# Kernel optimization log

Measured on AMD Instinct MI355X. Metric: run time of the kernel, lower is better.

The kernel has to match this reference:

```python
import jax, jax.numpy as jnp
import numpy as np

N_NODES = 50000
N_EDGES = 600000
F_IN = 64
N_GRAPHS = 2000
OUT_DIM = 1
BN_EPS = 1e-5


def _bn(x, gamma, beta):
    # BatchNorm1d training-mode forward: biased batch stats over node/row dim
    m = jnp.mean(x, axis=0)
    v = jnp.var(x, axis=0)
    return (x - m) * jax.lax.rsqrt(v + BN_EPS) * gamma + beta


def _gcn(x, W, b, src, dst):
    # PyG GCNConv: h = x @ W; symmetric-normalized aggregation with self-loops; bias after agg
    n = x.shape[0]
    h = x @ W                                    # [N, C_out]
    ones = jnp.ones((src.shape[0],), h.dtype)
    deg = jax.ops.segment_sum(ones, dst, num_segments=n) + 1.0  # +1 self-loop
    dinv = jax.lax.rsqrt(deg)
    norm = (dinv[src] * dinv[dst])[:, None]      # [E, 1]
    agg = jax.ops.segment_sum(h[src] * norm, dst, num_segments=n)
    agg = agg + h * (1.0 / deg)[:, None]         # self-loop term: deg^{-1/2}*deg^{-1/2}
    return agg + b


def _pool_mean(x, batch, g):
    s = jax.ops.segment_sum(x, batch, num_segments=g)
    c = jax.ops.segment_sum(jnp.ones((x.shape[0],), x.dtype), batch, num_segments=g)
    return s / jnp.maximum(c, 1.0)[:, None]


def _forward(xc, xs, W1c, b1c, g1c, be1c, W2c, b2c, g2c, be2c,
             W1s, b1s, g1s, be1s, W2s, b2s, g2s, be2s,
             Wf1, bf1, gf1, bef1, Wf2, bf2,
             src_c, dst_c, src_s, dst_s, batch):
    hc = jax.nn.relu(_bn(_gcn(xc, W1c, b1c, src_c, dst_c), g1c, be1c))
    hc = jax.nn.relu(_bn(_gcn(hc, W2c, b2c, src_c, dst_c), g2c, be2c))
    hs = jax.nn.relu(_bn(_gcn(xs, W1s, b1s, src_s, dst_s), g1s, be1s))
    hs = jax.nn.relu(_bn(_gcn(hs, W2s, b2s, src_s, dst_s), g2s, be2s))
    pc = _pool_mean(hc, batch, N_GRAPHS)         # [G, 64]
    ps = _pool_mean(hs, batch, N_GRAPHS)         # [G, 64]
    h = jnp.concatenate([pc, ps], axis=1)        # [G, 128]
    h = jax.nn.relu(_bn(h @ Wf1 + bf1, gf1, bef1))  # dropout is identity in eval
    return h @ Wf2 + bf2                         # [G, OUT_DIM]


def setup_inputs() -> dict:
    key = jax.random.key(0)
    ks = jax.random.split(key, 16)

    def glorot(k, fan_in, fan_out):
        s = np.sqrt(2.0 / (fan_in + fan_out)).astype(np.float32)
        return jax.random.normal(k, (fan_in, fan_out), jnp.float32) * s

    inp = {
        'x_chromophore': jax.random.normal(ks[0], (N_NODES, F_IN), jnp.float32),
        'x_solvent': jax.random.normal(ks[1], (N_NODES, F_IN), jnp.float32),
        'edge_index_chromophore': jax.random.randint(ks[2], (2, N_EDGES), 0, N_NODES),
        'edge_index_solvent': jax.random.randint(ks[3], (2, N_EDGES), 0, N_NODES),
        'batch': jnp.sort(jax.random.randint(ks[4], (N_NODES,), 0, N_GRAPHS)),
        # chromophore branch params
        'W1c': glorot(ks[5], F_IN, 128), 'b1c': jnp.zeros((128,), jnp.float32),
        'g1c': jnp.ones((128,), jnp.float32), 'be1c': jnp.zeros((128,), jnp.float32),
        'W2c': glorot(ks[6], 128, 64), 'b2c': jnp.zeros((64,), jnp.float32),
        'g2c': jnp.ones((64,), jnp.float32), 'be2c': jnp.zeros((64,), jnp.float32),
        # solvent branch params
        'W1s': glorot(ks[7], F_IN, 128), 'b1s': jnp.zeros((128,), jnp.float32),
        'g1s': jnp.ones((128,), jnp.float32), 'be1s': jnp.zeros((128,), jnp.float32),
        'W2s': glorot(ks[8], 128, 64), 'b2s': jnp.zeros((64,), jnp.float32),
        'g2s': jnp.ones((64,), jnp.float32), 'be2s': jnp.zeros((64,), jnp.float32),
        # MLP head
        'Wf1': glorot(ks[9], 128, 64), 'bf1': jnp.zeros((64,), jnp.float32),
        'gf1': jnp.ones((64,), jnp.float32), 'bef1': jnp.zeros((64,), jnp.float32),
        'Wf2': glorot(ks[10], 64, OUT_DIM), 'bf2': jnp.zeros((OUT_DIM,), jnp.float32),
    }
    return inp


def reference(x_chromophore, x_solvent, edge_index_chromophore, edge_index_solvent, batch,
              W1c, b1c, g1c, be1c, W2c, b2c, g2c, be2c,
              W1s, b1s, g1s, be1s, W2s, b2s, g2s, be2s,
              Wf1, bf1, gf1, bef1, Wf2, bf2):
    src_c, dst_c = edge_index_chromophore[0], edge_index_chromophore[1]
    src_s, dst_s = edge_index_solvent[0], edge_index_solvent[1]
    return _forward(x_chromophore, x_solvent,
                    W1c, b1c, g1c, be1c, W2c, b2c, g2c, be2c,
                    W1s, b1s, g1s, be1s, W2s, b2s, g2s, be2s,
                    Wf1, bf1, gf1, bef1, Wf2, bf2,
                    src_c, dst_c, src_s, dst_s, batch)
```

## Files before the change

### kernel.cpp

```cpp
#include <hip/hip_runtime.h>
#include <hip/hip_bf16.h>
#include <cstdint>
#include <cstddef>

#define NN 50000
#define NE 600000
#define NG 2000
#define NBUCK 49
#define SLOTS 16
#define NCHUNK 3125

typedef __attribute__((ext_vector_type(8))) short bf8;
typedef __attribute__((ext_vector_type(4))) float f32x4;

__device__ __forceinline__ unsigned short f2bf(float f) {
    uint32_t u = __float_as_uint(f);
    uint32_t r = (u + 0x7FFFu + ((u >> 16) & 1u)) >> 16;
    return (unsigned short)r;
}
__device__ __forceinline__ float bf2f(unsigned short h) {
    return __uint_as_float(((uint32_t)h) << 16);
}

__global__ __launch_bounds__(256) void conv_bf16_kernel(const float* __restrict__ x0,
                                                        const float* __restrict__ x1,
                                                        unsigned short* __restrict__ out) {
    int b = blockIdx.y;
    const float* x = b ? x1 : x0;
    unsigned short* o = out + (size_t)b * NN * 64;
    int i = (blockIdx.x * 256 + threadIdx.x) * 4;
    if (i + 3 < NN * 64) {
        float4 v = *(const float4*)&x[i];
        ushort4 r = make_ushort4(f2bf(v.x), f2bf(v.y), f2bf(v.z), f2bf(v.w));
        *(ushort4*)&o[i] = r;
    }
}

template<int K, int N>
__global__ __launch_bounds__(256) void pack_w(const float* __restrict__ W0,
                                              const float* __restrict__ W1,
                                              unsigned short* __restrict__ out) {
    int b = blockIdx.y;
    const float* W = b ? W1 : W0;
    unsigned short* o = out + (size_t)b * K * N;
    int idx = blockIdx.x * 256 + threadIdx.x;
    const int total = (N / 16) * (K / 32) * 64;
    if (idx >= total) return;
    int l = idx & 63;
    int th = idx >> 6;
    int h = th % (K / 32);
    int t = th / (K / 32);
    int col = t * 16 + (l & 15);
    int k0 = h * 32 + (l >> 4) * 8;
    ushort4 lo = make_ushort4(f2bf(W[(k0 + 0) * N + col]), f2bf(W[(k0 + 1) * N + col]),
                              f2bf(W[(k0 + 2) * N + col]), f2bf(W[(k0 + 3) * N + col]));
    ushort4 hi = make_ushort4(f2bf(W[(k0 + 4) * N + col]), f2bf(W[(k0 + 5) * N + col]),
                              f2bf(W[(k0 + 6) * N + col]), f2bf(W[(k0 + 7) * N + col]));
    *(ushort4*)&o[idx * 8] = lo;
    *(ushort4*)&o[idx * 8 + 4] = hi;
}

__global__ __launch_bounds__(256) void bucket_hist(const int* __restrict__ d0,
                                                   const int* __restrict__ d1,
                                                   int* __restrict__ bucketCnt, int nE) {
    int b = blockIdx.y;
    const int* dst = b ? d1 : d0;
    __shared__ int h[NBUCK];
    for (int i = threadIdx.x; i < NBUCK; i += 256) h[i] = 0;
    __syncthreads();
    for (int e = blockIdx.x * 256 + threadIdx.x; e < nE; e += gridDim.x * 256)
        atomicAdd(&h[dst[e] >> 10], 1);
    __syncthreads();
    for (int i = threadIdx.x; i < NBUCK; i += 256)
        if (h[i]) atomicAdd(&bucketCnt[b * NBUCK + i], h[i]);
}

__global__ void bucket_scan(const int* __restrict__ bucketCnt,
                            int* __restrict__ bucketOff, int* __restrict__ bucketCur) {
    int b = threadIdx.x;
    if (b < 2) {
        int run = 0;
        for (int i = 0; i < NBUCK; ++i) {
            bucketOff[b * NBUCK + i] = run;
            bucketCur[b * NBUCK + i] = run;
            run += bucketCnt[b * NBUCK + i];
        }
    }
}

__global__ __launch_bounds__(256) void bucket_scatter(const int* __restrict__ s0,
                                                      const int* __restrict__ d0,
                                                      const int* __restrict__ s1,
                                                      const int* __restrict__ d1,
                                                      int* __restrict__ bucketCur,
                                                      uint32_t* __restrict__ bent, int nE) {
    int b = blockIdx.y;
    const int* src = b ? s1 : s0;
    const int* dst = b ? d1 : d0;
    __shared__ int cnt[NBUCK];
    __shared__ int base[NBUCK];
    const int tid = threadIdx.x;
    for (int i = tid; i < NBUCK; i += 256) cnt[i] = 0;
    __syncthreads();

    const int e0 = blockIdx.x * 2048 + tid;
    int bk[8], slot[8];
    uint32_t pay[8];
#pragma unroll
    for (int k = 0; k < 8; ++k) {
        int e = e0 + k * 256;
        if (e < nE) {
            int d = dst[e], s = src[e];
            bk[k] = d >> 10;
            pay[k] = ((uint32_t)(d & 1023) << 16) | (uint32_t)s;
            slot[k] = atomicAdd(&cnt[bk[k]], 1);
        } else bk[k] = -1;
    }
    __syncthreads();
    for (int i = tid; i < NBUCK; i += 256) {
        int c = cnt[i];
        base[i] = c ? atomicAdd(&bucketCur[b * NBUCK + i], c) : 0;
    }
    __syncthreads();
#pragma unroll
    for (int k = 0; k < 8; ++k)
        if (bk[k] >= 0)
            bent[(size_t)b * NE + base[bk[k]] + slot[k]] = pay[k];
}

__global__ __launch_bounds__(256) void csr_build(const uint32_t* __restrict__ bent,
                                                 const int* __restrict__ bucketOff,
                                                 const int* __restrict__ bucketCnt,
                                                 int* __restrict__ row_ptr,
                                                 float* __restrict__ dinv,
                                                 uint16_t* __restrict__ perm) {
    __shared__ int lcnt[1024];
    __shared__ int lcur[1024];
    __shared__ int sscan[256];
    const int bk = blockIdx.x;
    const int b = blockIdx.y;
    const int tid = threadIdx.x;
    const int ebase = bucketOff[b * NBUCK + bk];
    const int ecnt = bucketCnt[b * NBUCK + bk];
    const int node0 = bk << 10;
    const uint32_t* be = bent + (size_t)b * NE + ebase;
    int* rp = row_ptr + b * (NN + 1);
    float* dv = dinv + (size_t)b * NN;
    uint16_t* pm = perm + (size_t)b * NE + ebase;

    for (int i = tid; i < 1024; i += 256) lcnt[i] = 0;
    __syncthreads();
    for (int i = tid; i < ecnt; i += 256) atomicAdd(&lcnt[be[i] >> 16], 1);
    __syncthreads();

    int c[4], s = 0;
#pragma unroll
    for (int j = 0; j < 4; ++j) { c[j] = lcnt[tid * 4 + j]; s += c[j]; }
    sscan[tid] = s;
    __syncthreads();
    for (int off = 1; off < 256; off <<= 1) {
        int v = (tid >= off) ? sscan[tid - off] : 0;
        __syncthreads();
        sscan[tid] += v;
        __syncthreads();
    }
    int run = sscan[tid] - s;
#pragma unroll
    for (int j = 0; j < 4; ++j) {
        int nl = tid * 4 + j;
        int g = node0 + nl;
        if (g < NN) {
            rp[g] = ebase + run;
            lcur[nl] = run;
            dv[g] = rsqrtf((float)c[j] + 1.0f);
        }
        run += c[j];
    }
    if (bk == NBUCK - 1 && tid == 0) rp[NN] = ebase + ecnt;
    __syncthreads();

    for (int i = tid; i < ecnt; i += 256) {
        uint32_t en = be[i];
        int nl = en >> 16;
        int pos = atomicAdd(&lcur[nl], 1);
        pm[pos] = (uint16_t)(en & 0xFFFFu);
    }
}

__global__ __launch_bounds__(256) void weight_fill(const uint16_t* __restrict__ perm,
                                                   const float* __restrict__ dinv,
                                                   uint32_t* __restrict__ permw, int nE) {
    int b = blockIdx.y;
    const uint16_t* pm = perm + (size_t)b * NE;
    const float* dv = dinv + (size_t)b * NN;
    uint32_t* pw = permw + (size_t)b * NE;
    int i = (blockIdx.x * 256 + threadIdx.x) * 4;
    if (i + 3 < nE) {
        ushort4 s4 = *(const ushort4*)&pm[i];
        uint4 o;
        o.x = ((uint32_t)f2bf(dv[s4.x]) << 16) | (uint32_t)s4.x;
        o.y = ((uint32_t)f2bf(dv[s4.y]) << 16) | (uint32_t)s4.y;
        o.z = ((uint32_t)f2bf(dv[s4.z]) << 16) | (uint32_t)s4.z;
        o.w = ((uint32_t)f2bf(dv[s4.w]) << 16) | (uint32_t)s4.w;
        *(uint4*)&pw[i] = o;
    } else {
        for (; i < nE; ++i) {
            uint16_t s = pm[i];
            pw[i] = ((uint32_t)f2bf(dv[s]) << 16) | (uint32_t)s;
        }
    }
}

__global__ __launch_bounds__(256) void gemm1_mfma(const unsigned short* __restrict__ Xbf,
                                                  const unsigned short* __restrict__ Wp,
                                                  unsigned short* __restrict__ Y) {
    const int b = blockIdx.y;
    const unsigned short* __restrict__ X = Xbf + (size_t)b * NN * 64;
    const unsigned short* __restrict__ W = Wp + (size_t)b * 64 * 128;
    unsigned short* __restrict__ Yb = Y + (size_t)b * NN * 128;
    const int tid = threadIdx.x;
    const int w = tid >> 6, lane = tid & 63;
    const int chunk = blockIdx.x * 4 + w;
    if (chunk >= NCHUNK) return;
    const int m = lane & 15, quad = lane >> 4;

    const int row = chunk * 16 + m;
    bf8 a0 = *(const bf8*)&X[(size_t)row * 64 + quad * 8];
    bf8 a1 = *(const bf8*)&X[(size_t)row * 64 + 32 + quad * 8];
    f32x4 acc[8];
#pragma unroll
    for (int t = 0; t < 8; ++t) acc[t] = (f32x4){0.f, 0.f, 0.f, 0.f};
#pragma unroll
    for (int t = 0; t < 8; ++t) {
        bf8 b0 = *(const bf8*)&W[((t * 2 + 0) * 64 + lane) * 8];
        bf8 b1 = *(const bf8*)&W[((t * 2 + 1) * 64 + lane) * 8];
        acc[t] = __builtin_amdgcn_mfma_f32_16x16x32_bf16(b0, a0, acc[t], 0, 0, 0);
        acc[t] = __builtin_amdgcn_mfma_f32_16x16x32_bf16(b1, a1, acc[t], 0, 0, 0);
    }
#pragma unroll
    for (int t = 0; t < 8; ++t) {
        uint32_t lo = (uint32_t)f2bf(acc[t][0]) | ((uint32_t)f2bf(acc[t][1]) << 16);
        uint32_t hi = (uint32_t)f2bf(acc[t][2]) | ((uint32_t)f2bf(acc[t][3]) << 16);
        *(uint2*)&Yb[(size_t)row * 128 + t * 16 + quad * 4] = make_uint2(lo, hi);
    }
}

__global__ __launch_bounds__(256) void stats128_bf16(const unsigned short* __restrict__ Y,
                                                     float* __restrict__ sums) {
    const int b = blockIdx.y;
    const unsigned short* __restrict__ Yb = Y + (size_t)b * NN * 128;
    const int g = threadIdx.x & 31;
    const int rs = threadIdx.x >> 5;
    float s0 = 0.f, s1 = 0.f, s2 = 0.f, s3 = 0.f;
    float q0 = 0.f, q1 = 0.f, q2 = 0.f, q3 = 0.f;
    for (int r = blockIdx.x * 8 + rs; r < NN; r += gridDim.x * 8) {
        uint2 v = *(const uint2*)&Yb[(size_t)r * 128 + g * 4];
        float x0 = __uint_as_float(v.x << 16);
        float x1 = __uint_as_float(v.x & 0xFFFF0000u);
        float x2 = __uint_as_float(v.y << 16);
        float x3 = __uint_as_float(v.y & 0xFFFF0000u);
        s0 += x0; s1 += x1; s2 += x2; s3 += x3;
        q0 = fmaf(x0, x0, q0); q1 = fmaf(x1, x1, q1);
        q2 = fmaf(x2, x2, q2); q3 = fmaf(x3, x3, q3);
    }
    __shared__ float ls[8][128], lq[8][128];
    *(float4*)&ls[rs][g * 4] = make_float4(s0, s1, s2, s3);
    *(float4*)&lq[rs][g * 4] = make_float4(q0, q1, q2, q3);
    __syncthreads();
    if (threadIdx.x < 128) {
        const int c = threadIdx.x;
        float S = 0.f, Q = 0.f;
#pragma unroll
        for (int k = 0; k < 8; ++k) { S += ls[k][c]; Q += lq[k][c]; }
        int slot = blockIdx.x & (SLOTS - 1);
        float* sb = sums + (size_t)(b * SLOTS + slot) * 256;
        atomicAdd(&sb[c], S);
        atomicAdd(&sb[128 + c], Q);
    }
}

__global__ __launch_bounds__(256) void gemm2_mfma(const unsigned short* __restrict__ H1,
                                                  const unsigned short* __restrict__ Wp,
                                                  const float* __restrict__ sums,
                                                  const float* __restrict__ g0,
                                                  const float* __restrict__ g1,
                                                  const float* __restrict__ be0,
                                                  const float* __restrict__ be1,
                                                  unsigned short* __restrict__ Y) {
    __shared__ float scLds[128], shLds[128];
    const int b = blockIdx.y;
    const unsigned short* __restrict__ X = H1 + (size_t)b * NN * 128;
    const unsigned short* __restrict__ W = Wp + (size_t)b * 128 * 64;
    unsigned short* __restrict__ Yb = Y + (size_t)b * NN * 64;
    const int tid = threadIdx.x;

    if (tid < 128) {
        float s = 0.f, s2 = 0.f;
#pragma unroll
        for (int k = 0; k < SLOTS; ++k) {
            const float* sb = sums + (size_t)(b * SLOTS + k) * 256;
            s += sb[tid];
            s2 += sb[128 + tid];
        }
        const float invN = 1.0f / (float)NN;
        float mean = s * invN;
        float var = s2 * invN - mean * mean;
        float gamma = b ? g1[tid] : g0[tid];
        float beta = b ? be1[tid] : be0[tid];
        float sc = gamma * rsqrtf(var + 1e-5f);
        scLds[tid] = sc;
        shLds[tid] = beta - mean * sc;
    }
    __syncthreads();

    const int w = tid >> 6, lane = tid & 63;
    const int chunk = blockIdx.x * 4 + w;
    if (chunk >= NCHUNK) return;
    const int m = lane & 15, quad = lane >> 4;
    const int row = chunk * 16 + m;

    f32x4 acc[4];
#pragma unroll
    for (int t = 0; t < 4; ++t) acc[t] = (f32x4){0.f, 0.f, 0.f, 0.f};
#pragma unroll
    for (int h = 0; h < 4; ++h) {
        const int k0 = h * 32 + quad * 8;
        bf8 araw = *(const bf8*)&X[(size_t)row * 128 + k0];
        float4 sc0 = *(const float4*)&scLds[k0];
        float4 sc1 = *(const float4*)&scLds[k0 + 4];
        float4 sh0 = *(const float4*)&shLds[k0];
        float4 sh1 = *(const float4*)&shLds[k0 + 4];
        float scv[8] = {sc0.x, sc0.y, sc0.z, sc0.w, sc1.x, sc1.y, sc1.z, sc1.w};
        float shv[8] = {sh0.x, sh0.y, sh0.z, sh0.w, sh1.x, sh1.y, sh1.z, sh1.w};
        bf8 af;
#pragma unroll
        for (int j = 0; j < 8; ++j) {
            float v = bf2f((unsigned short)araw[j]);
            v = fmaxf(fmaf(v, scv[j], shv[j]), 0.f);
            af[j] = (short)f2bf(v);
        }
#pragma unroll
        for (int t = 0; t < 4; ++t) {
            bf8 bf = *(const bf8*)&W[((t * 4 + h) * 64 + lane) * 8];
            acc[t] = __builtin_amdgcn_mfma_f32_16x16x32_bf16(bf, af, acc[t], 0, 0, 0);
        }
    }
#pragma unroll
    for (int t = 0; t < 4; ++t) {
        uint32_t lo = (uint32_t)f2bf(acc[t][0]) | ((uint32_t)f2bf(acc[t][1]) << 16);
        uint32_t hi = (uint32_t)f2bf(acc[t][2]) | ((uint32_t)f2bf(acc[t][3]) << 16);
        *(uint2*)&Yb[(size_t)row * 64 + t * 16 + quad * 4] = make_uint2(lo, hi);
    }
}

template<bool STATS>
__global__ __launch_bounds__(256) void agg2_kernel(const unsigned short* __restrict__ hall,
                                                   const int* __restrict__ row_ptr,
                                                   const uint32_t* __restrict__ permw,
                                                   const float* __restrict__ dinv,
                                                   unsigned short* __restrict__ out,
                                                   float* __restrict__ sums, int nNodes) {
    const int b = blockIdx.y;
    const unsigned short* __restrict__ h = hall + (size_t)b * NN * 64;
    const int* rp = row_ptr + b * (NN + 1);
    const uint32_t* pe = permw + (size_t)b * NE;
    const float* dv = dinv + (size_t)b * NN;
    unsigned short* ob = out + (size_t)b * nNodes * 64;

    const int w = threadIdx.x >> 6;
    const int wave = blockIdx.x * 4 + w;
    const int lane = threadIdx.x & 63;
    const int q = lane & 15;
    const int r = lane >> 4;
    float f0 = 0.f, f1 = 0.f, f2 = 0.f, f3 = 0.f;
    const bool active = wave < nNodes;
    if (active) {
        const int d = wave;
        const float di = dv[d];
        const int p0 = rp[d], p1 = rp[d + 1];
        float a0 = 0.f, a1 = 0.f, a2 = 0.f, a3 = 0.f;
        for (int p = p0; p < p1; p += 16) {
            uint32_t en[4];
#pragma unroll
            for (int k = 0; k < 4; ++k) {
                int e = p + k * 4 + r;
                bool vld = e < p1;
                en[k] = pe[vld ? e : p0];
                if (!vld) en[k] &= 0xFFFFu;
            }
#pragma unroll
            for (int k = 0; k < 4; ++k) {
                const int idx = (int)(en[k] & 0xFFFFu);
                const float wk = __uint_as_float(en[k] & 0xFFFF0000u);
                const uint2 hv = *(const uint2*)&h[(size_t)idx * 64 + q * 4];
                a0 = fmaf(wk, __uint_as_float(hv.x << 16), a0);
                a1 = fmaf(wk, __uint_as_float(hv.x & 0xFFFF0000u), a1);
                a2 = fmaf(wk, __uint_as_float(hv.y << 16), a2);
                a3 = fmaf(wk, __uint_as_float(hv.y & 0xFFFF0000u), a3);
            }
        }
        a0 += __shfl_xor(a0, 16, 64); a0 += __shfl_xor(a0, 32, 64);
        a1 += __shfl_xor(a1, 16, 64); a1 += __shfl_xor(a1, 32, 64);
        a2 += __shfl_xor(a2, 16, 64); a2 += __shfl_xor(a2, 32, 64);
        a3 += __shfl_xor(a3, 16, 64); a3 += __shfl_xor(a3, 32, 64);
        const uint2 sv = *(const uint2*)&h[(size_t)d * 64 + q * 4];
        f0 = di * fmaf(di, __uint_as_float(sv.x << 16), a0);
        f1 = di * fmaf(di, __uint_as_float(sv.x & 0xFFFF0000u), a1);
        f2 = di * fmaf(di, __uint_as_float(sv.y << 16), a2);
        f3 = di * fmaf(di, __uint_as_float(sv.y & 0xFFFF0000u), a3);
        if (r == 0) {
            uint32_t o0 = (uint32_t)f2bf(f0) | ((uint32_t)f2bf(f1) << 16);
            uint32_t o1 = (uint32_t)f2bf(f2) | ((uint32_t)f2bf(f3) << 16);
            *(uint2*)&ob[(size_t)d * 64 + q * 4] = make_uint2(o0, o1);
        }
    }
    if constexpr (STATS) {
        __shared__ float ls[256], ls2[256];
        if (lane < 16) {
            *(float4*)&ls[w * 64 + q * 4]  = make_float4(f0, f1, f2, f3);
            *(float4*)&ls2[w * 64 + q * 4] = make_float4(f0 * f0, f1 * f1, f2 * f2, f3 * f3);
        }
        __syncthreads();
        if (threadIdx.x < 64) {
            const int t = threadIdx.x;
            float s  = ls[t]  + ls[t + 64]  + ls[t + 128]  + ls[t + 192];
            float s2 = ls2[t] + ls2[t + 64] + ls2[t + 128] + ls2[t + 192];
            int slot = blockIdx.x & (SLOTS - 1);
            float* sb = sums + ((size_t)(b * SLOTS + slot) * 2) * 64;
            atomicAdd(&sb[t], s);
            atomicAdd(&sb[64 + t], s2);
        }
    }
}

__global__ __launch_bounds__(64) void pool2_kernel(const unsigned short* __restrict__ x,
                                                   const float* __restrict__ sums,
                                                   const float* __restrict__ g0,
                                                   const float* __restrict__ g1,
                                                   const float* __restrict__ be0,
                                                   const float* __restrict__ be1,
                                                   const int* __restrict__ batch,
                                                   float* __restrict__ Hmean, int n) {
    int b = blockIdx.y;
    const unsigned short* xb = x + (size_t)b * NN * 64;
    int g = blockIdx.x;
    int c = threadIdx.x;
    float s0 = 0.f, s20 = 0.f;
#pragma unroll
    for (int k = 0; k < SLOTS; ++k) {
        const float* sb = sums + ((size_t)(b * SLOTS + k) * 2) * 64;
        s0 += sb[c];
        s20 += sb[64 + c];
    }
    const float invN = 1.0f / (float)NN;
    float mean = s0 * invN;
    float var = s20 * invN - mean * mean;
    float gamma = b ? g1[c] : g0[c];
    float beta = b ? be1[c] : be0[c];
    float sc = gamma * rsqrtf(var + 1e-5f);
    float sh = beta - mean * sc;

    int lo = 0, hi = n;
    while (lo < hi) { int mid = (lo + hi) >> 1; if (batch[mid] < g) lo = mid + 1; else hi = mid; }
    int start = lo;
    hi = n;
    while (lo < hi) { int mid = (lo + hi) >> 1; if (batch[mid] <= g) lo = mid + 1; else hi = mid; }
    int end = lo;
    float s = 0.f;
    for (int r = start; r < end; ++r)
        s += fmaxf(fmaf(bf2f(xb[(size_t)r * 64 + c]), sc, sh), 0.f);
    float cf = (float)(end - start);
    Hmean[(size_t)g * 128 + b * 64 + c] = s / fmaxf(cf, 1.f);
}

__global__ __launch_bounds__(64) void head_gemm1_kernel(const float* __restrict__ H,
                                                        const float* __restrict__ Wf1,
                                                        float* __restrict__ T) {
    __shared__ float row[128];
    int g = blockIdx.x;
    int c = threadIdx.x;
    row[c] = H[(size_t)g * 128 + c];
    row[c + 64] = H[(size_t)g * 128 + 64 + c];
    __syncthreads();
    float acc = 0.f;
#pragma unroll 8
    for (int k = 0; k < 128; ++k) acc = fmaf(row[k], Wf1[k * 64 + c], acc);
    T[(size_t)g * 64 + c] = acc;
}

template<int C>
__global__ __launch_bounds__(256) void bn_stats_kernel(const float* __restrict__ x, int n,
                                                       float* __restrict__ sums) {
    constexpr int RP = 256 / C;
    __shared__ float ls[256], ls2[256];
    int c = threadIdx.x % C;
    int sub = threadIdx.x / C;
    float s = 0.f, s2 = 0.f;
    for (int r = blockIdx.x * RP + sub; r < n; r += gridDim.x * RP) {
        float v = x[(size_t)r * C + c];
        s += v; s2 += v * v;
    }
    ls[threadIdx.x] = s; ls2[threadIdx.x] = s2;
    __syncthreads();
    if (sub == 0) {
#pragma unroll
        for (int k = 1; k < RP; ++k) { s += ls[k * C + c]; s2 += ls2[k * C + c]; }
        atomicAdd(&sums[c], s);
        atomicAdd(&sums[C + c], s2);
    }
}

__global__ __launch_bounds__(64) void head_final_kernel(const float* __restrict__ T,
                                                        const float* __restrict__ hsums,
                                                        const float* __restrict__ gf1,
                                                        const float* __restrict__ bef1,
                                                        const float* __restrict__ Wf2,
                                                        const float* __restrict__ bf2,
                                                        float* __restrict__ out) {
    int g = blockIdx.x;
    int c = threadIdx.x;
    const float invG = 1.0f / (float)NG;
    float mean = hsums[c] * invG;
    float var = hsums[64 + c] * invG - mean * mean;
    float sc = gf1[c] * rsqrtf(var + 1e-5f);
    float sh = bef1[c] - mean * sc;
    float v = fmaxf(fmaf(T[(size_t)g * 64 + c], sc, sh), 0.f) * Wf2[c];
#pragma unroll
    for (int off = 32; off > 0; off >>= 1) v += __shfl_down(v, off, 64);
    if (c == 0) out[g] = v + bf2[0];
}


static inline size_t alignup(size_t x) { return (x + 255) & ~(size_t)255; }

extern "C" void kernel_launch(void* const* d_in, const int* in_sizes, int n_in,
                              void* d_out, int out_size, void* d_ws, size_t ws_size,
                              hipStream_t stream) {
    const float* xc  = (const float*)d_in[0];
    const float* xs  = (const float*)d_in[1];
    const int*   eic = (const int*)d_in[2];
    const int*   eis = (const int*)d_in[3];
    const int*   batch = (const int*)d_in[4];
    const float* W1c = (const float*)d_in[5];
    const float* g1c = (const float*)d_in[7];
    const float* be1c = (const float*)d_in[8];
    const float* W2c = (const float*)d_in[9];
    const float* g2c = (const float*)d_in[11];
    const float* be2c = (const float*)d_in[12];
    const float* W1s = (const float*)d_in[13];
    const float* g1s = (const float*)d_in[15];
    const float* be1s = (const float*)d_in[16];
    const float* W2s = (const float*)d_in[17];
    const float* g2s = (const float*)d_in[19];
    const float* be2s = (const float*)d_in[20];
    const float* Wf1 = (const float*)d_in[21];
    const float* gf1 = (const float*)d_in[23];
    const float* bef1 = (const float*)d_in[24];
    const float* Wf2 = (const float*)d_in[25];
    const float* bf2 = (const float*)d_in[26];
    float* out = (float*)d_out;

    char* ws = (char*)d_ws;
    size_t off = 0;
    auto alloc = [&](size_t bytes) { char* p = ws + off; off += alignup(bytes); return p; };

    int*      bucketCnt = (int*)alloc(2 * NBUCK * 4);
    int*      bucketOff = (int*)alloc(2 * NBUCK * 4);
    int*      bucketCur = (int*)alloc(2 * NBUCK * 4);
    uint32_t* bent      = (uint32_t*)alloc((size_t)2 * NE * 4);
    uint16_t* perm      = (uint16_t*)alloc(((size_t)2 * NE + 64) * 2);
    int*      row_ptr   = (int*)alloc(2 * (NN + 1) * 4);
    float*    dinv      = (float*)alloc((size_t)2 * NN * 4);
    unsigned short* xbf   = (unsigned short*)alloc((size_t)2 * NN * 64 * 2);
    unsigned short* aggbf = (unsigned short*)alloc((size_t)2 * NN * 64 * 2);
    unsigned short* h1bf  = (unsigned short*)alloc((size_t)2 * NN * 128 * 2);
    unsigned short* h2bf  = (unsigned short*)alloc((size_t)2 * NN * 64 * 2);
    unsigned short* Wp1   = (unsigned short*)alloc((size_t)2 * 64 * 128 * 2);
    unsigned short* Wp2   = (unsigned short*)alloc((size_t)2 * 128 * 64 * 2);
    float*    sums1     = (float*)alloc(((size_t)2 * SLOTS * 256 + (size_t)2 * SLOTS * 128 + 128) * 4);
    float*    sums2     = sums1 + (size_t)2 * SLOTS * 256;
    float*    hsums     = sums2 + (size_t)2 * SLOTS * 128;
    float*    Hmean     = (float*)alloc((size_t)NG * 128 * 4);
    float*    T         = (float*)alloc((size_t)NG * 64 * 4);

    const size_t statBytes = ((size_t)2 * SLOTS * 256 + (size_t)2 * SLOTS * 128 + 128) * 4;
    const int gemmBlocks = (NCHUNK + 3) / 4;
    const int aggBlocks = (NN + 3) / 4;

    conv_bf16_kernel<<<dim3((NN * 64 / 4 + 255) / 256, 2), 256, 0, stream>>>(xc, xs, xbf);
    pack_w<64, 128><<<dim3(4, 2), 256, 0, stream>>>(W1c, W1s, Wp1);
    pack_w<128, 64><<<dim3(4, 2), 256, 0, stream>>>(W2c, W2s, Wp2);
    hipMemsetAsync(sums1, 0, statBytes, stream);

    hipMemsetAsync(bucketCnt, 0, 2 * NBUCK * 4, stream);
    bucket_hist<<<dim3(64, 2), 256, 0, stream>>>(eic + NE, eis + NE, bucketCnt, NE);
    bucket_scan<<<1, 64, 0, stream>>>(bucketCnt, bucketOff, bucketCur);
    bucket_scatter<<<dim3((NE + 2047) / 2048, 2), 256, 0, stream>>>(
        eic, eic + NE, eis, eis + NE, bucketCur, bent, NE);
    csr_build<<<dim3(NBUCK, 2), 256, 0, stream>>>(bent, bucketOff, bucketCnt,
                                                  row_ptr, dinv, perm);
    weight_fill<<<dim3((NE / 4 + 255) / 256, 2), 256, 0, stream>>>(perm, dinv, bent, NE);

    agg2_kernel<false><<<dim3(aggBlocks, 2), 256, 0, stream>>>(
        xbf, row_ptr, bent, dinv, aggbf, nullptr, NN);
    gemm1_mfma<<<dim3(gemmBlocks, 2), 256, 0, stream>>>(aggbf, Wp1, h1bf);
    stats128_bf16<<<dim3(256, 2), 256, 0, stream>>>(h1bf, sums1);

    gemm2_mfma<<<dim3(gemmBlocks, 2), 256, 0, stream>>>(h1bf, Wp2, sums1,
                                                        g1c, g1s, be1c, be1s, h2bf);
    agg2_kernel<true><<<dim3(aggBlocks, 2), 256, 0, stream>>>(
        h2bf, row_ptr, bent, dinv, aggbf, sums2, NN);

    pool2_kernel<<<dim3(NG, 2), 64, 0, stream>>>(aggbf, sums2, g2c, g2s, be2c, be2s,
                                                 batch, Hmean, NN);

    head_gemm1_kernel<<<NG, 64, 0, stream>>>(Hmean, Wf1, T);
    bn_stats_kernel<64><<<32, 256, 0, stream>>>(T, NG, hsums);
    head_final_kernel<<<NG, 64, 0, stream>>>(T, hsums, gf1, bef1, Wf2, bf2, out);
}
```

Measured before the change: 354.6 us.

## Pad CSR rows to multiples of 16 and widen aggregation gathers to 16-byte loads

Each node's CSR row is padded to a multiple of 16 entries. Padding slots carry a zero weight and index 0, so the aggregation loop needs no bounds checks. Row pointers become (start,end) int2 pairs. The aggregation kernel now has 8 lanes per row, each loading 8 bf16 features with uint4, and 8 rows are gathered per iteration, followed by a three-step shuffle reduction. The cost is extra padded edge storage, padded work in weight_fill and on low-degree nodes, and more serial padding writes in csr_build.

```diff
diff --git a/kernel.cpp b/kernel.cpp
--- a/kernel.cpp
+++ b/kernel.cpp
@@ -9,6 +9,7 @@
 #define NBUCK 49
 #define SLOTS 16
 #define NCHUNK 3125
+#define PNE (NE + NBUCK * 15 * 1024)
 
 typedef __attribute__((ext_vector_type(8))) short bf8;
 typedef __attribute__((ext_vector_type(4))) float f32x4;
@@ -21,6 +22,8 @@
 __device__ __forceinline__ float bf2f(unsigned short h) {
     return __uint_as_float(((uint32_t)h) << 16);
 }
+__device__ __forceinline__ float lo16(uint32_t v) { return __uint_as_float(v << 16); }
+__device__ __forceinline__ float hi16(uint32_t v) { return __uint_as_float(v & 0xFFFF0000u); }
 
 __global__ __launch_bounds__(256) void conv_bf16_kernel(const float* __restrict__ x0,
                                                         const float* __restrict__ x1,
@@ -125,13 +128,13 @@
 #pragma unroll
     for (int k = 0; k < 8; ++k)
         if (bk[k] >= 0)
-            bent[(size_t)b * NE + base[bk[k]] + slot[k]] = pay[k];
+            bent[(size_t)b * (size_t)PNE + base[bk[k]] + slot[k]] = pay[k];
 }
 
 __global__ __launch_bounds__(256) void csr_build(const uint32_t* __restrict__ bent,
                                                  const int* __restrict__ bucketOff,
                                                  const int* __restrict__ bucketCnt,
-                                                 int* __restrict__ row_ptr,
+                                                 int2* __restrict__ rpe,
                                                  float* __restrict__ dinv,
                                                  uint16_t* __restrict__ perm) {
     __shared__ int lcnt[1024];
@@ -142,20 +145,25 @@
     const int tid = threadIdx.x;
     const int ebase = bucketOff[b * NBUCK + bk];
     const int ecnt = bucketCnt[b * NBUCK + bk];
+    const int P0 = ebase + bk * 15360;
     const int node0 = bk << 10;
-    const uint32_t* be = bent + (size_t)b * NE + ebase;
-    int* rp = row_ptr + b * (NN + 1);
+    const uint32_t* be = bent + (size_t)b * (size_t)PNE + ebase;
+    int2* rp = rpe + (size_t)b * NN;
     float* dv = dinv + (size_t)b * NN;
-    uint16_t* pm = perm + (size_t)b * NE + ebase;
+    uint16_t* pm = perm + (size_t)b * (size_t)PNE + P0;
 
     for (int i = tid; i < 1024; i += 256) lcnt[i] = 0;
     __syncthreads();
     for (int i = tid; i < ecnt; i += 256) atomicAdd(&lcnt[be[i] >> 16], 1);
     __syncthreads();
 
-    int c[4], s = 0;
-#pragma unroll
-    for (int j = 0; j < 4; ++j) { c[j] = lcnt[tid * 4 + j]; s += c[j]; }
+    int c[4], pc[4], s = 0;
+#pragma unroll
+    for (int j = 0; j < 4; ++j) {
+        c[j] = lcnt[tid * 4 + j];
+        pc[j] = (c[j] + 15) & ~15;
+        s += pc[j];
+    }
     sscan[tid] = s;
     __syncthreads();
     for (int off = 1; off < 256; off <<= 1) {
@@ -170,13 +178,12 @@
         int nl = tid * 4 + j;
         int g = node0 + nl;
         if (g < NN) {
-            rp[g] = ebase + run;
+            rp[g] = make_int2(P0 + run, P0 + run + pc[j]);
             lcur[nl] = run;
             dv[g] = rsqrtf((float)c[j] + 1.0f);
         }
-        run += c[j];
-    }
-    if (bk == NBUCK - 1 && tid == 0) rp[NN] = ebase + ecnt;
+        run += pc[j];
+    }
     __syncthreads();
 
     for (int i = tid; i < ecnt; i += 256) {
@@ -185,28 +192,38 @@
         int pos = atomicAdd(&lcur[nl], 1);
         pm[pos] = (uint16_t)(en & 0xFFFFu);
     }
+    __syncthreads();
+
+    int run2 = sscan[tid] - s;
+#pragma unroll
+    for (int j = 0; j < 4; ++j) {
+        int g = node0 + tid * 4 + j;
+        if (g < NN)
+            for (int t = c[j]; t < pc[j]; ++t) pm[run2 + t] = 0xFFFFu;
+        run2 += pc[j];
+    }
 }
 
 __global__ __launch_bounds__(256) void weight_fill(const uint16_t* __restrict__ perm,
                                                    const float* __restrict__ dinv,
                                                    uint32_t* __restrict__ permw, int nE) {
     int b = blockIdx.y;
-    const uint16_t* pm = perm + (size_t)b * NE;
+    const uint16_t* pm = perm + (size_t)b * (size_t)PNE;
     const float* dv = dinv + (size_t)b * NN;
-    uint32_t* pw = permw + (size_t)b * NE;
+    uint32_t* pw = permw + (size_t)b * (size_t)PNE;
     int i = (blockIdx.x * 256 + threadIdx.x) * 4;
     if (i + 3 < nE) {
         ushort4 s4 = *(const ushort4*)&pm[i];
         uint4 o;
-        o.x = ((uint32_t)f2bf(dv[s4.x]) << 16) | (uint32_t)s4.x;
-        o.y = ((uint32_t)f2bf(dv[s4.y]) << 16) | (uint32_t)s4.y;
-        o.z = ((uint32_t)f2bf(dv[s4.z]) << 16) | (uint32_t)s4.z;
-        o.w = ((uint32_t)f2bf(dv[s4.w]) << 16) | (uint32_t)s4.w;
+        o.x = (s4.x < NN) ? (((uint32_t)f2bf(dv[s4.x]) << 16) | (uint32_t)s4.x) : 0u;
+        o.y = (s4.y < NN) ? (((uint32_t)f2bf(dv[s4.y]) << 16) | (uint32_t)s4.y) : 0u;
+        o.z = (s4.z < NN) ? (((uint32_t)f2bf(dv[s4.z]) << 16) | (uint32_t)s4.z) : 0u;
+        o.w = (s4.w < NN) ? (((uint32_t)f2bf(dv[s4.w]) << 16) | (uint32_t)s4.w) : 0u;
         *(uint4*)&pw[i] = o;
     } else {
         for (; i < nE; ++i) {
             uint16_t s = pm[i];
-            pw[i] = ((uint32_t)f2bf(dv[s]) << 16) | (uint32_t)s;
+            pw[i] = (s < NN) ? (((uint32_t)f2bf(dv[s]) << 16) | (uint32_t)s) : 0u;
         }
     }
 }
@@ -255,10 +272,10 @@
     float q0 = 0.f, q1 = 0.f, q2 = 0.f, q3 = 0.f;
     for (int r = blockIdx.x * 8 + rs; r < NN; r += gridDim.x * 8) {
         uint2 v = *(const uint2*)&Yb[(size_t)r * 128 + g * 4];
-        float x0 = __uint_as_float(v.x << 16);
-        float x1 = __uint_as_float(v.x & 0xFFFF0000u);
-        float x2 = __uint_as_float(v.y << 16);
-        float x3 = __uint_as_float(v.y & 0xFFFF0000u);
+        float x0 = lo16(v.x);
+        float x1 = hi16(v.x);
+        float x2 = lo16(v.y);
+        float x3 = hi16(v.y);
         s0 += x0; s1 += x1; s2 += x2; s3 += x3;
         q0 = fmaf(x0, x0, q0); q1 = fmaf(x1, x1, q1);
         q2 = fmaf(x2, x2, q2); q3 = fmaf(x3, x3, q3);
@@ -355,70 +372,90 @@
 
 template<bool STATS>
 __global__ __launch_bounds__(256) void agg2_kernel(const unsigned short* __restrict__ hall,
-                                                   const int* __restrict__ row_ptr,
+                                                   const int2* __restrict__ rpe,
                                                    const uint32_t* __restrict__ permw,
                                                    const float* __restrict__ dinv,
                                                    unsigned short* __restrict__ out,
                                                    float* __restrict__ sums, int nNodes) {
     const int b = blockIdx.y;
     const unsigned short* __restrict__ h = hall + (size_t)b * NN * 64;
-    const int* rp = row_ptr + b * (NN + 1);
-    const uint32_t* pe = permw + (size_t)b * NE;
+    const int2* rp = rpe + (size_t)b * NN;
+    const uint32_t* pe = permw + (size_t)b * (size_t)PNE;
     const float* dv = dinv + (size_t)b * NN;
     unsigned short* ob = out + (size_t)b * nNodes * 64;
 
     const int w = threadIdx.x >> 6;
     const int wave = blockIdx.x * 4 + w;
     const int lane = threadIdx.x & 63;
-    const int q = lane & 15;
-    const int r = lane >> 4;
-    float f0 = 0.f, f1 = 0.f, f2 = 0.f, f3 = 0.f;
+    const int g = lane >> 3;
+    const int c = lane & 7;
+    float a0 = 0.f, a1 = 0.f, a2 = 0.f, a3 = 0.f;
+    float a4 = 0.f, a5 = 0.f, a6 = 0.f, a7 = 0.f;
+    float fv[8];
+#pragma unroll
+    for (int j = 0; j < 8; ++j) fv[j] = 0.f;
+
     const bool active = wave < nNodes;
     if (active) {
         const int d = wave;
         const float di = dv[d];
-        const int p0 = rp[d], p1 = rp[d + 1];
-        float a0 = 0.f, a1 = 0.f, a2 = 0.f, a3 = 0.f;
-        for (int p = p0; p < p1; p += 16) {
-            uint32_t en[4];
-#pragma unroll
-            for (int k = 0; k < 4; ++k) {
-                int e = p + k * 4 + r;
-                bool vld = e < p1;
-                en[k] = pe[vld ? e : p0];
-                if (!vld) en[k] &= 0xFFFFu;
-            }
-#pragma unroll
-            for (int k = 0; k < 4; ++k) {
-                const int idx = (int)(en[k] & 0xFFFFu);
-                const float wk = __uint_as_float(en[k] & 0xFFFF0000u);
-                const uint2 hv = *(const uint2*)&h[(size_t)idx * 64 + q * 4];
-                a0 = fmaf(wk, __uint_as_float(hv.x << 16), a0);
-                a1 = fmaf(wk, __uint_as_float(hv.x & 0xFFFF0000u), a1);
-                a2 = fmaf(wk, __uint_as_float(hv.y << 16), a2);
-                a3 = fmaf(wk, __uint_as_float(hv.y & 0xFFFF0000u), a3);
-            }
-        }
-        a0 += __shfl_xor(a0, 16, 64); a0 += __shfl_xor(a0, 32, 64);
-        a1 += __shfl_xor(a1, 16, 64); a1 += __shfl_xor(a1, 32, 64);
-        a2 += __shfl_xor(a2, 16, 64); a2 += __shfl_xor(a2, 32, 64);
-        a3 += __shfl_xor(a3, 16, 64); a3 += __shfl_xor(a3, 32, 64);
-        const uint2 sv = *(const uint2*)&h[(size_t)d * 64 + q * 4];
-        f0 = di * fmaf(di, __uint_as_float(sv.x << 16), a0);
-        f1 = di * fmaf(di, __uint_as_float(sv.x & 0xFFFF0000u), a1);
-        f2 = di * fmaf(di, __uint_as_float(sv.y << 16), a2);
-        f3 = di * fmaf(di, __uint_as_float(sv.y & 0xFFFF0000u), a3);
-        if (r == 0) {
-            uint32_t o0 = (uint32_t)f2bf(f0) | ((uint32_t)f2bf(f1) << 16);
-            uint32_t o1 = (uint32_t)f2bf(f2) | ((uint32_t)f2bf(f3) << 16);
-            *(uint2*)&ob[(size_t)d * 64 + q * 4] = make_uint2(o0, o1);
+        const int2 pr = rp[d];
+        for (int p = pr.x; p < pr.y; p += 16) {
+            const uint32_t e0 = pe[p + g];
+            const uint32_t e1 = pe[p + 8 + g];
+            const int i0 = (int)(e0 & 0xFFFFu);
+            const int i1 = (int)(e1 & 0xFFFFu);
+            const float w0 = __uint_as_float(e0 & 0xFFFF0000u);
+            const float w1 = __uint_as_float(e1 & 0xFFFF0000u);
+            const uint4 v0 = *(const uint4*)&h[(size_t)i0 * 64 + c * 8];
+            const uint4 v1 = *(const uint4*)&h[(size_t)i1 * 64 + c * 8];
+            a0 = fmaf(w0, lo16(v0.x), a0); a1 = fmaf(w0, hi16(v0.x), a1);
+            a2 = fmaf(w0, lo16(v0.y), a2); a3 = fmaf(w0, hi16(v0.y), a3);
+            a4 = fmaf(w0, lo16(v0.z), a4); a5 = fmaf(w0, hi16(v0.z), a5);
+            a6 = fmaf(w0, lo16(v0.w), a6); a7 = fmaf(w0, hi16(v0.w), a7);
+            a0 = fmaf(w1, lo16(v1.x), a0); a1 = fmaf(w1, hi16(v1.x), a1);
+            a2 = fmaf(w1, lo16(v1.y), a2); a3 = fmaf(w1, hi16(v1.y), a3);
+            a4 = fmaf(w1, lo16(v1.z), a4); a5 = fmaf(w1, hi16(v1.z), a5);
+            a6 = fmaf(w1, lo16(v1.w), a6); a7 = fmaf(w1, hi16(v1.w), a7);
+        }
+        a0 += __shfl_xor(a0, 8, 64);  a1 += __shfl_xor(a1, 8, 64);
+        a2 += __shfl_xor(a2, 8, 64);  a3 += __shfl_xor(a3, 8, 64);
+        a4 += __shfl_xor(a4, 8, 64);  a5 += __shfl_xor(a5, 8, 64);
+        a6 += __shfl_xor(a6, 8, 64);  a7 += __shfl_xor(a7, 8, 64);
+        a0 += __shfl_xor(a0, 16, 64); a1 += __shfl_xor(a1, 16, 64);
+        a2 += __shfl_xor(a2, 16, 64); a3 += __shfl_xor(a3, 16, 64);
+        a4 += __shfl_xor(a4, 16, 64); a5 += __shfl_xor(a5, 16, 64);
+        a6 += __shfl_xor(a6, 16, 64); a7 += __shfl_xor(a7, 16, 64);
+        a0 += __shfl_xor(a0, 32, 64); a1 += __shfl_xor(a1, 32, 64);
+        a2 += __shfl_xor(a2, 32, 64); a3 += __shfl_xor(a3, 32, 64);
+        a4 += __shfl_xor(a4, 32, 64); a5 += __shfl_xor(a5, 32, 64);
+        a6 += __shfl_xor(a6, 32, 64); a7 += __shfl_xor(a7, 32, 64);
+
+        if (g == 0) {
+            const uint4 sv = *(const uint4*)&h[(size_t)d * 64 + c * 8];
+            fv[0] = di * fmaf(di, lo16(sv.x), a0);
+            fv[1] = di * fmaf(di, hi16(sv.x), a1);
+            fv[2] = di * fmaf(di, lo16(sv.y), a2);
+            fv[3] = di * fmaf(di, hi16(sv.y), a3);
+            fv[4] = di * fmaf(di, lo16(sv.z), a4);
+            fv[5] = di * fmaf(di, hi16(sv.z), a5);
+            fv[6] = di * fmaf(di, lo16(sv.w), a6);
+            fv[7] = di * fmaf(di, hi16(sv.w), a7);
+            uint4 o;
+            o.x = (uint32_t)f2bf(fv[0]) | ((uint32_t)f2bf(fv[1]) << 16);
+            o.y = (uint32_t)f2bf(fv[2]) | ((uint32_t)f2bf(fv[3]) << 16);
+            o.z = (uint32_t)f2bf(fv[4]) | ((uint32_t)f2bf(fv[5]) << 16);
+            o.w = (uint32_t)f2bf(fv[6]) | ((uint32_t)f2bf(fv[7]) << 16);
+            *(uint4*)&ob[(size_t)d * 64 + c * 8] = o;
         }
     }
     if constexpr (STATS) {
         __shared__ float ls[256], ls2[256];
-        if (lane < 16) {
-            *(float4*)&ls[w * 64 + q * 4]  = make_float4(f0, f1, f2, f3);
-            *(float4*)&ls2[w * 64 + q * 4] = make_float4(f0 * f0, f1 * f1, f2 * f2, f3 * f3);
+        if (g == 0) {
+            *(float4*)&ls[w * 64 + c * 8]      = make_float4(fv[0], fv[1], fv[2], fv[3]);
+            *(float4*)&ls[w * 64 + c * 8 + 4]  = make_float4(fv[4], fv[5], fv[6], fv[7]);
+            *(float4*)&ls2[w * 64 + c * 8]     = make_float4(fv[0]*fv[0], fv[1]*fv[1], fv[2]*fv[2], fv[3]*fv[3]);
+            *(float4*)&ls2[w * 64 + c * 8 + 4] = make_float4(fv[4]*fv[4], fv[5]*fv[5], fv[6]*fv[6], fv[7]*fv[7]);
         }
         __syncthreads();
         if (threadIdx.x < 64) {
@@ -567,9 +604,9 @@
     int*      bucketCnt = (int*)alloc(2 * NBUCK * 4);
     int*      bucketOff = (int*)alloc(2 * NBUCK * 4);
     int*      bucketCur = (int*)alloc(2 * NBUCK * 4);
-    uint32_t* bent      = (uint32_t*)alloc((size_t)2 * NE * 4);
-    uint16_t* perm      = (uint16_t*)alloc(((size_t)2 * NE + 64) * 2);
-    int*      row_ptr   = (int*)alloc(2 * (NN + 1) * 4);
+    uint32_t* bent      = (uint32_t*)alloc((size_t)2 * PNE * 4);
+    uint16_t* perm      = (uint16_t*)alloc(((size_t)2 * PNE + 64) * 2);
+    int2*     rpe       = (int2*)alloc((size_t)2 * NN * 8);
     float*    dinv      = (float*)alloc((size_t)2 * NN * 4);
     unsigned short* xbf   = (unsigned short*)alloc((size_t)2 * NN * 64 * 2);
     unsigned short* aggbf = (unsigned short*)alloc((size_t)2 * NN * 64 * 2);
@@ -598,18 +635,18 @@
     bucket_scatter<<<dim3((NE + 2047) / 2048, 2), 256, 0, stream>>>(
         eic, eic + NE, eis, eis + NE, bucketCur, bent, NE);
     csr_build<<<dim3(NBUCK, 2), 256, 0, stream>>>(bent, bucketOff, bucketCnt,
-                                                  row_ptr, dinv, perm);
-    weight_fill<<<dim3((NE / 4 + 255) / 256, 2), 256, 0, stream>>>(perm, dinv, bent, NE);
+                                                  rpe, dinv, perm);
+    weight_fill<<<dim3((PNE / 4 + 255) / 256, 2), 256, 0, stream>>>(perm, dinv, bent, PNE);
 
     agg2_kernel<false><<<dim3(aggBlocks, 2), 256, 0, stream>>>(
-        xbf, row_ptr, bent, dinv, aggbf, nullptr, NN);
+        xbf, rpe, bent, dinv, aggbf, nullptr, NN);
     gemm1_mfma<<<dim3(gemmBlocks, 2), 256, 0, stream>>>(aggbf, Wp1, h1bf);
     stats128_bf16<<<dim3(256, 2), 256, 0, stream>>>(h1bf, sums1);
 
     gemm2_mfma<<<dim3(gemmBlocks, 2), 256, 0, stream>>>(h1bf, Wp2, sums1,
                                                         g1c, g1s, be1c, be1s, h2bf);
     agg2_kernel<true><<<dim3(aggBlocks, 2), 256, 0, stream>>>(
-        h2bf, row_ptr, bent, dinv, aggbf, sums2, NN);
+        h2bf, rpe, bent, dinv, aggbf, sums2, NN);
 
     pool2_kernel<<<dim3(NG, 2), 64, 0, stream>>>(aggbf, sums2, g2c, g2s, be2c, be2s,
                                                  batch, Hmean, NN);
```

Result: no change. 359.2 us (+1.3%).

## Sort CSR neighbor lists in LDS and precompute graph node ranges

Applied to the files above, without the earlier changes.

In csr_build, each bucket's permuted source indices are now staged in a shared-memory buffer. Each thread then insertion-sorts the neighbor lists of its rows before writing them out, which makes the gathers in aggregation read rows in ascending order and should improve cache locality. A new graph_ranges kernel computes start and end node indices per graph once, replacing two binary searches per pool block. The cost is extra serial sorting work in csr_build, a 32KB LDS buffer that can limit occupancy, and an added kernel launch plus memset. The pooling change assumes batch is sorted and treats graphs with no nodes as empty via the memset.

```diff
diff --git a/kernel.cpp b/kernel.cpp
--- a/kernel.cpp
+++ b/kernel.cpp
@@ -21,6 +21,8 @@
 __device__ __forceinline__ float bf2f(unsigned short h) {
     return __uint_as_float(((uint32_t)h) << 16);
 }
+__device__ __forceinline__ float lo16(uint32_t v) { return __uint_as_float(v << 16); }
+__device__ __forceinline__ float hi16(uint32_t v) { return __uint_as_float(v & 0xFFFF0000u); }
 
 __global__ __launch_bounds__(256) void conv_bf16_kernel(const float* __restrict__ x0,
                                                         const float* __restrict__ x1,
@@ -137,6 +139,7 @@
     __shared__ int lcnt[1024];
     __shared__ int lcur[1024];
     __shared__ int sscan[256];
+    __shared__ uint16_t spm[16384];
     const int bk = blockIdx.x;
     const int b = blockIdx.y;
     const int tid = threadIdx.x;
@@ -179,11 +182,31 @@
     if (bk == NBUCK - 1 && tid == 0) rp[NN] = ebase + ecnt;
     __syncthreads();
 
+    const bool useLds = (ecnt <= 16384);
+    uint16_t* dstbuf = useLds ? spm : pm;
     for (int i = tid; i < ecnt; i += 256) {
         uint32_t en = be[i];
         int nl = en >> 16;
         int pos = atomicAdd(&lcur[nl], 1);
-        pm[pos] = (uint16_t)(en & 0xFFFFu);
+        dstbuf[pos] = (uint16_t)(en & 0xFFFFu);
+    }
+    __syncthreads();
+
+    if (useLds) {
+        int st = sscan[tid] - s;
+#pragma unroll
+        for (int j = 0; j < 4; ++j) {
+            const int cnt = c[j];
+            for (int a = st + 1; a < st + cnt; ++a) {
+                uint16_t v = spm[a];
+                int k2 = a - 1;
+                while (k2 >= st && spm[k2] > v) { spm[k2 + 1] = spm[k2]; --k2; }
+                spm[k2 + 1] = v;
+            }
+            st += cnt;
+        }
+        __syncthreads();
+        for (int i = tid; i < ecnt; i += 256) pm[i] = spm[i];
     }
 }
 
@@ -211,6 +234,16 @@
     }
 }
 
+__global__ __launch_bounds__(256) void graph_ranges(const int* __restrict__ batch,
+                                                    int* __restrict__ gstart,
+                                                    int* __restrict__ gend, int n) {
+    int i = blockIdx.x * 256 + threadIdx.x;
+    if (i >= n) return;
+    int g = batch[i];
+    if (i == 0 || batch[i - 1] != g) gstart[g] = i;
+    if (i == n - 1 || batch[i + 1] != g) gend[g] = i + 1;
+}
+
 __global__ __launch_bounds__(256) void gemm1_mfma(const unsigned short* __restrict__ Xbf,
                                                   const unsigned short* __restrict__ Wp,
                                                   unsigned short* __restrict__ Y) {
@@ -255,10 +288,10 @@
     float q0 = 0.f, q1 = 0.f, q2 = 0.f, q3 = 0.f;
     for (int r = blockIdx.x * 8 + rs; r < NN; r += gridDim.x * 8) {
         uint2 v = *(const uint2*)&Yb[(size_t)r * 128 + g * 4];
-        float x0 = __uint_as_float(v.x << 16);
-        float x1 = __uint_as_float(v.x & 0xFFFF0000u);
-        float x2 = __uint_as_float(v.y << 16);
-        float x3 = __uint_as_float(v.y & 0xFFFF0000u);
+        float x0 = lo16(v.x);
+        float x1 = hi16(v.x);
+        float x2 = lo16(v.y);
+        float x3 = hi16(v.y);
         s0 += x0; s1 += x1; s2 += x2; s3 += x3;
         q0 = fmaf(x0, x0, q0); q1 = fmaf(x1, x1, q1);
         q2 = fmaf(x2, x2, q2); q3 = fmaf(x3, x3, q3);
@@ -393,10 +426,10 @@
                 const int idx = (int)(en[k] & 0xFFFFu);
                 const float wk = __uint_as_float(en[k] & 0xFFFF0000u);
                 const uint2 hv = *(const uint2*)&h[(size_t)idx * 64 + q * 4];
-                a0 = fmaf(wk, __uint_as_float(hv.x << 16), a0);
-                a1 = fmaf(wk, __uint_as_float(hv.x & 0xFFFF0000u), a1);
-                a2 = fmaf(wk, __uint_as_float(hv.y << 16), a2);
-                a3 = fmaf(wk, __uint_as_float(hv.y & 0xFFFF0000u), a3);
+                a0 = fmaf(wk, lo16(hv.x), a0);
+                a1 = fmaf(wk, hi16(hv.x), a1);
+                a2 = fmaf(wk, lo16(hv.y), a2);
+                a3 = fmaf(wk, hi16(hv.y), a3);
             }
         }
         a0 += __shfl_xor(a0, 16, 64); a0 += __shfl_xor(a0, 32, 64);
@@ -404,10 +437,10 @@
         a2 += __shfl_xor(a2, 16, 64); a2 += __shfl_xor(a2, 32, 64);
         a3 += __shfl_xor(a3, 16, 64); a3 += __shfl_xor(a3, 32, 64);
         const uint2 sv = *(const uint2*)&h[(size_t)d * 64 + q * 4];
-        f0 = di * fmaf(di, __uint_as_float(sv.x << 16), a0);
-        f1 = di * fmaf(di, __uint_as_float(sv.x & 0xFFFF0000u), a1);
-        f2 = di * fmaf(di, __uint_as_float(sv.y << 16), a2);
-        f3 = di * fmaf(di, __uint_as_float(sv.y & 0xFFFF0000u), a3);
+        f0 = di * fmaf(di, lo16(sv.x), a0);
+        f1 = di * fmaf(di, hi16(sv.x), a1);
+        f2 = di * fmaf(di, lo16(sv.y), a2);
+        f3 = di * fmaf(di, hi16(sv.y), a3);
         if (r == 0) {
             uint32_t o0 = (uint32_t)f2bf(f0) | ((uint32_t)f2bf(f1) << 16);
             uint32_t o1 = (uint32_t)f2bf(f2) | ((uint32_t)f2bf(f3) << 16);
@@ -439,8 +472,9 @@
                                                    const float* __restrict__ g1,
                                                    const float* __restrict__ be0,
                                                    const float* __restrict__ be1,
-                                                   const int* __restrict__ batch,
-                                                   float* __restrict__ Hmean, int n) {
+                                                   const int* __restrict__ gstart,
+                                                   const int* __restrict__ gend,
+                                                   float* __restrict__ Hmean) {
     int b = blockIdx.y;
     const unsigned short* xb = x + (size_t)b * NN * 64;
     int g = blockIdx.x;
@@ -460,12 +494,8 @@
     float sc = gamma * rsqrtf(var + 1e-5f);
     float sh = beta - mean * sc;
 
-    int lo = 0, hi = n;
-    while (lo < hi) { int mid = (lo + hi) >> 1; if (batch[mid] < g) lo = mid + 1; else hi = mid; }
-    int start = lo;
-    hi = n;
-    while (lo < hi) { int mid = (lo + hi) >> 1; if (batch[mid] <= g) lo = mid + 1; else hi = mid; }
-    int end = lo;
+    int start = gstart[g];
+    int end = gend[g];
     float s = 0.f;
     for (int r = start; r < end; ++r)
         s += fmaxf(fmaf(bf2f(xb[(size_t)r * 64 + c]), sc, sh), 0.f);
@@ -571,6 +601,7 @@
     uint16_t* perm      = (uint16_t*)alloc(((size_t)2 * NE + 64) * 2);
     int*      row_ptr   = (int*)alloc(2 * (NN + 1) * 4);
     float*    dinv      = (float*)alloc((size_t)2 * NN * 4);
+    int*      gbound    = (int*)alloc((size_t)2 * NG * 4);
     unsigned short* xbf   = (unsigned short*)alloc((size_t)2 * NN * 64 * 2);
     unsigned short* aggbf = (unsigned short*)alloc((size_t)2 * NN * 64 * 2);
     unsigned short* h1bf  = (unsigned short*)alloc((size_t)2 * NN * 128 * 2);
@@ -582,6 +613,8 @@
     float*    hsums     = sums2 + (size_t)2 * SLOTS * 128;
     float*    Hmean     = (float*)alloc((size_t)NG * 128 * 4);
     float*    T         = (float*)alloc((size_t)NG * 64 * 4);
+    int*      gstart    = gbound;
+    int*      gend      = gbound + NG;
 
     const size_t statBytes = ((size_t)2 * SLOTS * 256 + (size_t)2 * SLOTS * 128 + 128) * 4;
     const int gemmBlocks = (NCHUNK + 3) / 4;
@@ -591,6 +624,8 @@
     pack_w<64, 128><<<dim3(4, 2), 256, 0, stream>>>(W1c, W1s, Wp1);
     pack_w<128, 64><<<dim3(4, 2), 256, 0, stream>>>(W2c, W2s, Wp2);
     hipMemsetAsync(sums1, 0, statBytes, stream);
+    hipMemsetAsync(gbound, 0, 2 * NG * 4, stream);
+    graph_ranges<<<(NN + 255) / 256, 256, 0, stream>>>(batch, gstart, gend, NN);
 
     hipMemsetAsync(bucketCnt, 0, 2 * NBUCK * 4, stream);
     bucket_hist<<<dim3(64, 2), 256, 0, stream>>>(eic + NE, eis + NE, bucketCnt, NE);
@@ -612,7 +647,7 @@
         h2bf, row_ptr, bent, dinv, aggbf, sums2, NN);
 
     pool2_kernel<<<dim3(NG, 2), 64, 0, stream>>>(aggbf, sums2, g2c, g2s, be2c, be2s,
-                                                 batch, Hmean, NN);
+                                                 gstart, gend, Hmean);
 
     head_gemm1_kernel<<<NG, 64, 0, stream>>>(Hmean, Wf1, T);
     bn_stats_kernel<64><<<32, 256, 0, stream>>>(T, NG, hsums);
```

New measurement: 421.8 us. 19.0% more time.
